# Kernel optimization log

Measured on AMD Instinct MI355X. Metric: run time of the kernel, lower is better.

Reference implementation:

```python
import jax, jax.numpy as jnp
import numpy as np

NEG_SLOPE = 0.2  # PyG GATConv default leaky_relu slope


def _gat_conv(x, src, dst, W, a_src, a_dst, b, num_nodes):
    # Linear transform: [N, F_out]
    h = x @ W
    # Per-node attention halves (heads=1): [N]
    alpha_s = h @ a_src
    alpha_d = h @ a_dst
    # Per-edge raw score for edge j->i: a_src.h_j + a_dst.h_i
    e = jax.nn.leaky_relu(alpha_s[src] + alpha_d[dst], NEG_SLOPE)
    # Softmax over edges grouped by destination node (numerically stable)
    m = jax.ops.segment_max(e, dst, num_segments=num_nodes)
    ex = jnp.exp(e - m[dst])
    denom = jax.ops.segment_sum(ex, dst, num_segments=num_nodes)
    coef = ex / denom[dst]
    # Attention-weighted aggregation of source features into destinations
    out = jax.ops.segment_sum(h[src] * coef[:, None], dst, num_segments=num_nodes)
    return out + b


def setup_inputs() -> dict:
    key = jax.random.key(0)
    ks = jax.random.split(key, 12)
    N, F_in, F_hid, F_out, E = 100000, 128, 64, 40, 1600000
    x = jax.random.normal(ks[0], (N, F_in), dtype=jnp.float32)
    edge_index = jax.random.randint(ks[1], (2, E), 0, N, dtype=jnp.int64)
    g = lambda k, shape, fan: jax.random.normal(k, shape, dtype=jnp.float32) * (1.0 / np.sqrt(fan))
    return {
        "x": x,
        "edge_index": edge_index,
        "W1": g(ks[2], (F_in, F_hid), F_in),
        "a_src1": g(ks[3], (F_hid,), F_hid),
        "a_dst1": g(ks[4], (F_hid,), F_hid),
        "b1": jnp.zeros((F_hid,), dtype=jnp.float32),
        "W2": g(ks[5], (F_hid, F_out), F_hid),
        "a_src2": g(ks[6], (F_out,), F_out),
        "a_dst2": g(ks[7], (F_out,), F_out),
        "b2": jnp.zeros((F_out,), dtype=jnp.float32),
    }


def reference(x, edge_index, W1, a_src1, a_dst1, b1, W2, a_src2, a_dst2, b2):
    N = x.shape[0]
    # PyG GATConv adds self loops by default
    loops = jnp.arange(N, dtype=edge_index.dtype)
    src = jnp.concatenate([edge_index[0], loops])
    dst = jnp.concatenate([edge_index[1], loops])
    h = _gat_conv(x, src, dst, W1, a_src1, a_dst1, b1, N)
    h = jax.nn.relu(h)
    # dropout p=0.5 is inactive in eval mode
    h = _gat_conv(h, src, dst, W2, a_src2, a_dst2, b2, N)
    return jax.nn.log_softmax(h, axis=-1)
```

## Files before the change

### kernel.cpp

```cpp
#include <hip/hip_runtime.h>
#include <math.h>


constexpr int F_IN = 128;
constexpr int F_H  = 64;
constexpr int F_O  = 40;
constexpr int NBMAX = 512;
constexpr int CHUNK = 8192;
constexpr int NKEY  = 2048;

using h2 = decltype(__builtin_amdgcn_cvt_pkrtz(0.f, 0.f));
typedef __attribute__((ext_vector_type(4))) float f32x4;
typedef __attribute__((ext_vector_type(8))) short s16x8;

__device__ __forceinline__ h2 u2h(unsigned u) { return __builtin_bit_cast(h2, u); }

__device__ __forceinline__ float fdot2f(h2 a, h2 b, float c) {
#if __has_builtin(__builtin_amdgcn_fdot2)
    return __builtin_amdgcn_fdot2(a, b, c, false);
#else
    return c + (float)a.x * (float)b.x + (float)a.y * (float)b.y;
#endif
}
__device__ __forceinline__ h2 pklo(unsigned a, unsigned b) {
    return u2h(__builtin_amdgcn_perm(a, b, 0x05040100u));
}
__device__ __forceinline__ h2 pkhi(unsigned a, unsigned b) {
    return u2h(__builtin_amdgcn_perm(a, b, 0x07060302u));
}
__device__ __forceinline__ unsigned short f2h(float f) {
    _Float16 x = (_Float16)f;
    return __builtin_bit_cast(unsigned short, x);
}
__device__ __forceinline__ void nt_storef4(float4* p, float4 v) {
    __builtin_nontemporal_store(v.x, &p->x);
    __builtin_nontemporal_store(v.y, &p->y);
    __builtin_nontemporal_store(v.z, &p->z);
    __builtin_nontemporal_store(v.w, &p->w);
}


__global__ __launch_bounds__(256) void k_binA(const int* __restrict__ dsts,
                                              int* __restrict__ bcnt,
                                              int E, int Et, int NB) {
    __shared__ int hist[NBMAX];
    for (int i = threadIdx.x; i < NB; i += 256) hist[i] = 0;
    __syncthreads();
    int e0 = blockIdx.x * 2048;
#pragma unroll
    for (int it = 0; it < 8; ++it) {
        int e = e0 + it * 256 + threadIdx.x;
        if (e < Et) {
            int d = (e < E) ? dsts[e] : (e - E);
            atomicAdd(&hist[d >> 8], 1);
        }
    }
    __syncthreads();
    for (int i = threadIdx.x; i < NB; i += 256) {
        int c = hist[i];
        if (c) atomicAdd(&bcnt[i], c);
    }
}

__global__ __launch_bounds__(NBMAX) void k_binB(const int* __restrict__ bcnt,
                                                int* __restrict__ bbase,
                                                int* __restrict__ bcur,
                                                int* __restrict__ rp,
                                                int NB, int N, int Et) {
    __shared__ int sc[NBMAX];
    int t = threadIdx.x;
    int v = (t < NB) ? bcnt[t] : 0;
    sc[t] = v; __syncthreads();
    int x = v;
    for (int o = 1; o < NBMAX; o <<= 1) {
        int y = (t >= o) ? sc[t - o] : 0;
        __syncthreads();
        x += y;
        sc[t] = x;
        __syncthreads();
    }
    if (t < NB) { int b = x - v; bbase[t] = b; bcur[t] = b; }
    if (t == 0) rp[N] = Et;
}

__global__ __launch_bounds__(256) void k_binC(const int* __restrict__ srcs,
                                              const int* __restrict__ dsts,
                                              int* __restrict__ bcur,
                                              unsigned* __restrict__ binned,
                                              int E, int Et, int NB) {
    __shared__ int hist[NBMAX];
    __shared__ int gbase[NBMAX];
    __shared__ int lcnt[NBMAX];
    int t = threadIdx.x;
    for (int i = t; i < NB; i += 256) hist[i] = 0;
    __syncthreads();
    int e0 = blockIdx.x * CHUNK;
#pragma unroll 4
    for (int it = 0; it < CHUNK / 256; ++it) {
        int e = e0 + it * 256 + t;
        if (e < Et) {
            int d = (e < E) ? dsts[e] : (e - E);
            atomicAdd(&hist[d >> 8], 1);
        }
    }
    __syncthreads();
    for (int i = t; i < NB; i += 256) {
        int c = hist[i];
        gbase[i] = c ? atomicAdd(&bcur[i], c) : 0;
        lcnt[i] = 0;
    }
    __syncthreads();
#pragma unroll 4
    for (int it = 0; it < CHUNK / 256; ++it) {
        int e = e0 + it * 256 + t;
        if (e < Et) {
            int s, d;
            if (e < E) { s = srcs[e]; d = dsts[e]; } else { s = e - E; d = s; }
            int b = d >> 8;
            int p = atomicAdd(&lcnt[b], 1);
            binned[gbase[b] + p] = (unsigned)s | ((unsigned)(d & 255) << 24);
        }
    }
}


__global__ __launch_bounds__(256) void k_binD(const unsigned* __restrict__ binned,
                                              const int* __restrict__ bbase,
                                              const int* __restrict__ bcur,
                                              int* __restrict__ rp,
                                              int* __restrict__ csr, int N) {
    __shared__ int hist[NKEY];
    __shared__ int sc2[NKEY];
    __shared__ int lcnt[NKEY];
    __shared__ int tsum[256];
    int b = blockIdx.x, t = threadIdx.x;
    int base = bbase[b], end = bcur[b];
    for (int k = t; k < NKEY; k += 256) { hist[k] = 0; lcnt[k] = 0; }
    __syncthreads();
    for (int j = base + t; j < end; j += 256) {
        unsigned w = binned[j];
        int key = ((int)(w >> 24) << 3) | (int)((w & 0xFFFFFFu) >> 14);
        atomicAdd(&hist[key], 1);
    }
    __syncthreads();
    int myk = t << 3;
    int s = 0;
#pragma unroll
    for (int k = 0; k < 8; ++k) s += hist[myk + k];
    tsum[t] = s; __syncthreads();
    int x = s;
    for (int o = 1; o < 256; o <<= 1) {
        int y = (t >= o) ? tsum[t - o] : 0;
        __syncthreads();
        x += y;
        tsum[t] = x;
        __syncthreads();
    }
    int run = x - s;
    int g = (b << 8) + t;
    if (g < N) rp[g] = base + run;
#pragma unroll
    for (int k = 0; k < 8; ++k) { sc2[myk + k] = run; run += hist[myk + k]; }
    __syncthreads();
    for (int j = base + t; j < end; j += 256) {
        unsigned w = binned[j];
        int src = (int)(w & 0xFFFFFFu);
        int key = ((int)(w >> 24) << 3) | (src >> 14);
        int p = atomicAdd(&lcnt[key], 1);
        csr[base + sc2[key] + p] = src;
    }
}


__global__ __launch_bounds__(256) void k_wsplit(const float* __restrict__ W,
                                                unsigned short* __restrict__ WhiT,
                                                unsigned short* __restrict__ WloT) {
    int i = blockIdx.x * 256 + threadIdx.x;
    if (i >= F_IN * F_H) return;
    int k = i >> 6, c = i & 63;
    float w = W[i];
    unsigned u = __float_as_uint(w);
    unsigned hi = u & 0xFFFF0000u;
    float d = w - __uint_as_float(hi);
    WhiT[c * F_IN + k] = (unsigned short)(hi >> 16);
    WloT[c * F_IN + k] = (unsigned short)(__float_as_uint(d) >> 16);
}


__global__ __launch_bounds__(256, 2) void k_gemm1m(const float* __restrict__ x,
                                                   const unsigned short* __restrict__ WhiT,
                                                   const unsigned short* __restrict__ WloT,
                                                   const float* __restrict__ avs,
                                                   const float* __restrict__ avd,
                                                   unsigned short* __restrict__ h,
                                                   float* __restrict__ as,
                                                   float* __restrict__ ad, int N) {
    __shared__ __align__(16) float xs[64][132];
    unsigned short (*hs)[72] = (unsigned short(*)[72])xs;
    const int t = threadIdx.x;
    const int wv = t >> 6;
    const int lane = t & 63;
    const int lrow = lane & 15;
    const int lk8 = lane >> 4;
    const int r0 = blockIdx.x * 64;

    {
        const float4* xg = (const float4*)x;
#pragma unroll
        for (int it = 0; it < 8; ++it) {
            int flat = it * 256 + t;
            int row = flat >> 5, c4 = flat & 31;
            int grow = min(r0 + row, N - 1);
            float4 v = xg[(size_t)grow * 32 + c4];
            *(float4*)&xs[row][c4 * 4] = v;
        }
    }

    s16x8 bh[4][4], bl[4][4];
#pragma unroll
    for (int kt = 0; kt < 4; ++kt)
#pragma unroll
        for (int ct = 0; ct < 4; ++ct) {
            const int boff = (ct * 16 + lrow) * F_IN + kt * 32 + lk8 * 8;
            bh[kt][ct] = *(const s16x8*)&WhiT[boff];
            bl[kt][ct] = *(const s16x8*)&WloT[boff];
        }
    __syncthreads();

    s16x8 ah[4], al[4];
#pragma unroll
    for (int kt = 0; kt < 4; ++kt) {
        const float* rp_ = &xs[wv * 16 + lrow][kt * 32 + lk8 * 8];
        float4 a = *(const float4*)rp_;
        float4 b = *(const float4*)(rp_ + 4);
        float e0[8] = {a.x, a.y, a.z, a.w, b.x, b.y, b.z, b.w};
        unsigned uh[4], ul[4];
#pragma unroll
        for (int p = 0; p < 4; ++p) {
            float a0 = e0[2 * p], a1 = e0[2 * p + 1];
            unsigned u0 = __float_as_uint(a0), u1 = __float_as_uint(a1);
            float d0 = a0 - __uint_as_float(u0 & 0xFFFF0000u);
            float d1 = a1 - __uint_as_float(u1 & 0xFFFF0000u);
            uh[p] = __builtin_amdgcn_perm(u1, u0, 0x07060302u);
            ul[p] = __builtin_amdgcn_perm(__float_as_uint(d1), __float_as_uint(d0), 0x07060302u);
        }
        ah[kt] = __builtin_bit_cast(s16x8, make_uint4(uh[0], uh[1], uh[2], uh[3]));
        al[kt] = __builtin_bit_cast(s16x8, make_uint4(ul[0], ul[1], ul[2], ul[3]));
    }
    __syncthreads();

    f32x4 acc[4] = {};
#pragma unroll
    for (int kt = 0; kt < 4; ++kt) {
#pragma unroll
        for (int ct = 0; ct < 4; ++ct) {
            acc[ct] = __builtin_amdgcn_mfma_f32_16x16x32_bf16(ah[kt], bh[kt][ct], acc[ct], 0, 0, 0);
            acc[ct] = __builtin_amdgcn_mfma_f32_16x16x32_bf16(al[kt], bh[kt][ct], acc[ct], 0, 0, 0);
            acc[ct] = __builtin_amdgcn_mfma_f32_16x16x32_bf16(ah[kt], bl[kt][ct], acc[ct], 0, 0, 0);
        }
    }

    float avs_c[4], avd_c[4];
#pragma unroll
    for (int ct = 0; ct < 4; ++ct) {
        avs_c[ct] = avs[ct * 16 + lrow];
        avd_c[ct] = avd[ct * 16 + lrow];
    }
#pragma unroll
    for (int r = 0; r < 4; ++r) {
        float ps = acc[0][r] * avs_c[0] + acc[1][r] * avs_c[1]
                 + acc[2][r] * avs_c[2] + acc[3][r] * avs_c[3];
        float pd = acc[0][r] * avd_c[0] + acc[1][r] * avd_c[1]
                 + acc[2][r] * avd_c[2] + acc[3][r] * avd_c[3];
#pragma unroll
        for (int o = 8; o; o >>= 1) {
            ps += __shfl_xor(ps, o, 16);
            pd += __shfl_xor(pd, o, 16);
        }
        int orow = r0 + wv * 16 + lk8 * 4 + r;
        if (lrow == 0 && orow < N) { as[orow] = ps; ad[orow] = pd; }
    }

#pragma unroll
    for (int ct = 0; ct < 4; ++ct)
#pragma unroll
        for (int r = 0; r < 4; ++r)
            hs[wv * 16 + lk8 * 4 + r][ct * 16 + lrow] = f2h(acc[ct][r]);
    __syncthreads();
    const int row = t >> 2, ch = t & 3;
    const int grow = r0 + row;
    if (grow < N) {
        uint4 v0 = *(const uint4*)&hs[row][ch * 16];
        uint4 v1 = *(const uint4*)&hs[row][ch * 16 + 8];
        uint4* gp = (uint4*)(h + (size_t)grow * F_H + ch * 16);
        gp[0] = v0; gp[1] = v1;
    }
}


__global__ __launch_bounds__(256) void k_gemm2(const unsigned short* __restrict__ xin,
                                               const float* __restrict__ W,
                                               const float* __restrict__ avs,
                                               const float* __restrict__ avd,
                                               unsigned short* __restrict__ h,
                                               float* __restrict__ as,
                                               float* __restrict__ ad, int N) {
    __shared__ __align__(16) float Ws[F_H * F_O];
    for (int i = threadIdx.x; i < F_H * F_O; i += 256) Ws[i] = W[i];
    __syncthreads();
    int t = threadIdx.x;
    int r0 = blockIdx.x * 64 + (t >> 3) * 2;
    int l = t & 7;
    if (r0 >= N) return;
    const uint2* xa = (const uint2*)(xin + (size_t)r0 * F_H);
    const uint2* xb = (const uint2*)(xin + (size_t)(r0 + 1) * F_H);
    float acca[5] = {}, accb[5] = {};
#pragma unroll
    for (int k4 = 0; k4 < F_H / 4; ++k4) {
        uint2 ua = xa[k4];
        uint2 ub = xb[k4];
        h2 a01 = u2h(ua.x), a23 = u2h(ua.y);
        h2 b01 = u2h(ub.x), b23 = u2h(ub.y);
        float xva[4] = {(float)a01.x, (float)a01.y, (float)a23.x, (float)a23.y};
        float xvb[4] = {(float)b01.x, (float)b01.y, (float)b23.x, (float)b23.y};
        int kb = k4 * 4;
#pragma unroll
        for (int kk = 0; kk < 4; ++kk) {
            const float* wr = &Ws[(kb + kk) * F_O + l];
            float w0 = wr[0], w1 = wr[8], w2 = wr[16], w3 = wr[24], w4 = wr[32];
            float xs = xva[kk];
            acca[0] += xs * w0; acca[1] += xs * w1; acca[2] += xs * w2;
            acca[3] += xs * w3; acca[4] += xs * w4;
            float ys = xvb[kk];
            accb[0] += ys * w0; accb[1] += ys * w1; accb[2] += ys * w2;
            accb[3] += ys * w3; accb[4] += ys * w4;
        }
    }
    float psa = 0.f, pda = 0.f, psb = 0.f, pdb = 0.f;
    unsigned short* ra = h + (size_t)r0 * F_H;
    unsigned short* rb = h + (size_t)(r0 + 1) * F_H;
#pragma unroll
    for (int cc = 0; cc < 5; ++cc) {
        int c = l + 8 * cc;
        ra[c] = f2h(acca[cc]);
        rb[c] = f2h(accb[cc]);
        float vs = avs[c], vd = avd[c];
        psa += acca[cc] * vs; pda += acca[cc] * vd;
        psb += accb[cc] * vs; pdb += accb[cc] * vd;
    }
#pragma unroll
    for (int pp = 0; pp < 3; ++pp) {
        int c = 40 + l * 3 + pp;
        ra[c] = 0; rb[c] = 0;
    }
#pragma unroll
    for (int o = 4; o; o >>= 1) {
        psa += __shfl_xor(psa, o, 8);
        pda += __shfl_xor(pda, o, 8);
        psb += __shfl_xor(psb, o, 8);
        pdb += __shfl_xor(pdb, o, 8);
    }
    if (l == 0) { as[r0] = psa; ad[r0] = pda; as[r0 + 1] = psb; ad[r0 + 1] = pdb; }
}


template <int FOUT, bool RELU, bool LOGSM, bool F16OUT>
__global__ __launch_bounds__(256) void k_agg(const int* __restrict__ rp,
                                             const int* __restrict__ csr,
                                             const float* __restrict__ as,
                                             const float* __restrict__ ad,
                                             const uint4* __restrict__ h4,
                                             const float* __restrict__ bias,
                                             void* __restrict__ outv, int N) {
    constexpr int CAP = 64;
    __shared__ __align__(16) uint2 wsb[4][8][CAP + 2];
    const int w = threadIdx.x >> 6;
    const int g = (threadIdx.x >> 3) & 7;
    const int c = threadIdx.x & 7;
    const int i = blockIdx.x * 32 + (threadIdx.x >> 3);
    if (i >= N) return;
    const int start = rp[i], end = rp[i + 1];
    const int deg = end - start;
    const int dm = min(deg, CAP);
    const int dmR8 = (dm + 7) & ~7;
    const float adi = ad[i];

    for (int idx = c; idx < dm; idx += 8) {
        int srcn = __builtin_nontemporal_load(&csr[start + idx]);
        float e = as[srcn] + adi;
        e = fmaxf(e, 0.2f * e);
        wsb[w][g][idx] = make_uint2(__float_as_uint(__expf(e)), (unsigned)srcn);
    }
    {
        int idx = dm + c;
        if (idx < dmR8) wsb[w][g][idx] = make_uint2(0u, (unsigned)i);
    }

    const uint4* pw = (const uint4*)wsb[w][g];
    float acc[8] = {}, acc2[8] = {};
    float sacc = 0.f;
    const int noct = dmR8 >> 3;
    for (int q = 0; q < noct; ++q) {
        uint4 m0 = pw[4 * q];
        uint4 m1 = pw[4 * q + 1];
        uint4 m2 = pw[4 * q + 2];
        uint4 m3 = pw[4 * q + 3];
        uint4 hv0 = h4[((size_t)m0.y << 3) + c];
        uint4 hv1 = h4[((size_t)m0.w << 3) + c];
        uint4 hv2 = h4[((size_t)m1.y << 3) + c];
        uint4 hv3 = h4[((size_t)m1.w << 3) + c];
        uint4 hv4 = h4[((size_t)m2.y << 3) + c];
        uint4 hv5 = h4[((size_t)m2.w << 3) + c];
        uint4 hv6 = h4[((size_t)m3.y << 3) + c];
        uint4 hv7 = h4[((size_t)m3.w << 3) + c];
        float w0 = __uint_as_float(m0.x), w1 = __uint_as_float(m0.z);
        float w2 = __uint_as_float(m1.x), w3 = __uint_as_float(m1.z);
        float w4 = __uint_as_float(m2.x), w5 = __uint_as_float(m2.z);
        float w6 = __uint_as_float(m3.x), w7 = __uint_as_float(m3.z);
        sacc += ((w0 + w1) + (w2 + w3)) + ((w4 + w5) + (w6 + w7));
        h2 wp0 = __builtin_amdgcn_cvt_pkrtz(w0, w1);
        h2 wp1 = __builtin_amdgcn_cvt_pkrtz(w2, w3);
        h2 wp2 = __builtin_amdgcn_cvt_pkrtz(w4, w5);
        h2 wp3 = __builtin_amdgcn_cvt_pkrtz(w6, w7);
        acc[0] = fdot2f(wp0, pklo(hv1.x, hv0.x), acc[0]);
        acc[1] = fdot2f(wp0, pkhi(hv1.x, hv0.x), acc[1]);
        acc[2] = fdot2f(wp0, pklo(hv1.y, hv0.y), acc[2]);
        acc[3] = fdot2f(wp0, pkhi(hv1.y, hv0.y), acc[3]);
        acc[4] = fdot2f(wp0, pklo(hv1.z, hv0.z), acc[4]);
        acc[5] = fdot2f(wp0, pkhi(hv1.z, hv0.z), acc[5]);
        acc[6] = fdot2f(wp0, pklo(hv1.w, hv0.w), acc[6]);
        acc[7] = fdot2f(wp0, pkhi(hv1.w, hv0.w), acc[7]);
        acc2[0] = fdot2f(wp1, pklo(hv3.x, hv2.x), acc2[0]);
        acc2[1] = fdot2f(wp1, pkhi(hv3.x, hv2.x), acc2[1]);
        acc2[2] = fdot2f(wp1, pklo(hv3.y, hv2.y), acc2[2]);
        acc2[3] = fdot2f(wp1, pkhi(hv3.y, hv2.y), acc2[3]);
        acc2[4] = fdot2f(wp1, pklo(hv3.z, hv2.z), acc2[4]);
        acc2[5] = fdot2f(wp1, pkhi(hv3.z, hv2.z), acc2[5]);
        acc2[6] = fdot2f(wp1, pklo(hv3.w, hv2.w), acc2[6]);
        acc2[7] = fdot2f(wp1, pkhi(hv3.w, hv2.w), acc2[7]);
        acc[0] = fdot2f(wp2, pklo(hv5.x, hv4.x), acc[0]);
        acc[1] = fdot2f(wp2, pkhi(hv5.x, hv4.x), acc[1]);
        acc[2] = fdot2f(wp2, pklo(hv5.y, hv4.y), acc[2]);
        acc[3] = fdot2f(wp2, pkhi(hv5.y, hv4.y), acc[3]);
        acc[4] = fdot2f(wp2, pklo(hv5.z, hv4.z), acc[4]);
        acc[5] = fdot2f(wp2, pkhi(hv5.z, hv4.z), acc[5]);
        acc[6] = fdot2f(wp2, pklo(hv5.w, hv4.w), acc[6]);
        acc[7] = fdot2f(wp2, pkhi(hv5.w, hv4.w), acc[7]);
        acc2[0] = fdot2f(wp3, pklo(hv7.x, hv6.x), acc2[0]);
        acc2[1] = fdot2f(wp3, pkhi(hv7.x, hv6.x), acc2[1]);
        acc2[2] = fdot2f(wp3, pklo(hv7.y, hv6.y), acc2[2]);
        acc2[3] = fdot2f(wp3, pkhi(hv7.y, hv6.y), acc2[3]);
        acc2[4] = fdot2f(wp3, pklo(hv7.z, hv6.z), acc2[4]);
        acc2[5] = fdot2f(wp3, pkhi(hv7.z, hv6.z), acc2[5]);
        acc2[6] = fdot2f(wp3, pklo(hv7.w, hv6.w), acc2[6]);
        acc2[7] = fdot2f(wp3, pkhi(hv7.w, hv6.w), acc2[7]);
    }

    for (int j = start + dm; j < end; ++j) {
        int srcn = __builtin_nontemporal_load(&csr[j]);
        float e = as[srcn] + adi;
        e = fmaxf(e, 0.2f * e);
        float wv = __expf(e);
        sacc += wv;
        uint4 hv = h4[((size_t)srcn << 3) + c];
        h2 wp = __builtin_amdgcn_cvt_pkrtz(wv, 0.f);
        acc[0] = fdot2f(wp, pklo(hv.x, hv.x), acc[0]);
        acc[1] = fdot2f(wp, pkhi(hv.x, hv.x), acc[1]);
        acc[2] = fdot2f(wp, pklo(hv.y, hv.y), acc[2]);
        acc[3] = fdot2f(wp, pkhi(hv.y, hv.y), acc[3]);
        acc[4] = fdot2f(wp, pklo(hv.z, hv.z), acc[4]);
        acc[5] = fdot2f(wp, pkhi(hv.z, hv.z), acc[5]);
        acc[6] = fdot2f(wp, pklo(hv.w, hv.w), acc[6]);
        acc[7] = fdot2f(wp, pkhi(hv.w, hv.w), acc[7]);
    }

#pragma unroll
    for (int k = 0; k < 8; ++k) acc[k] += acc2[k];
    float inv = 1.f / sacc;

    if (!LOGSM) {
        float r[8];
#pragma unroll
        for (int k = 0; k < 8; ++k) {
            r[k] = fmaf(acc[k], inv, bias[8 * c + k]);
            if (RELU) r[k] = fmaxf(r[k], 0.f);
        }
        if (F16OUT) {
            unsigned short* oh = (unsigned short*)outv;
            unsigned u0 = (unsigned)f2h(r[0]) | ((unsigned)f2h(r[1]) << 16);
            unsigned u1 = (unsigned)f2h(r[2]) | ((unsigned)f2h(r[3]) << 16);
            unsigned u2 = (unsigned)f2h(r[4]) | ((unsigned)f2h(r[5]) << 16);
            unsigned u3 = (unsigned)f2h(r[6]) | ((unsigned)f2h(r[7]) << 16);
            *(uint4*)(oh + (size_t)i * F_H + 8 * c) = make_uint4(u0, u1, u2, u3);
        } else {
            float* out = (float*)outv;
            float4* op = (float4*)(out + (size_t)i * FOUT + 8 * c);
            nt_storef4(op, make_float4(r[0], r[1], r[2], r[3]));
            nt_storef4(op + 1, make_float4(r[4], r[5], r[6], r[7]));
        }
    } else {
        float* out = (float*)outv;
        constexpr int VC = FOUT / 8;
        bool act = (c < VC);
        float v[8];
#pragma unroll
        for (int k = 0; k < 8; ++k) {
            float bv = bias[act ? 8 * c + k : 0];
            v[k] = act ? fmaf(acc[k], inv, bv) : -INFINITY;
        }
        float mx = v[0];
#pragma unroll
        for (int k = 1; k < 8; ++k) mx = fmaxf(mx, v[k]);
#pragma unroll
        for (int o = 1; o <= 4; o <<= 1) mx = fmaxf(mx, __shfl_xor(mx, o));
        float es = 0.f;
        if (act) {
#pragma unroll
            for (int k = 0; k < 8; ++k) es += __expf(v[k] - mx);
        }
#pragma unroll
        for (int o = 1; o <= 4; o <<= 1) es += __shfl_xor(es, o);
        if (act) {
            float lse = mx + __logf(es);
            float4* op = (float4*)(out + (size_t)i * FOUT + 8 * c);
            nt_storef4(op, make_float4(v[0] - lse, v[1] - lse, v[2] - lse, v[3] - lse));
            nt_storef4(op + 1, make_float4(v[4] - lse, v[5] - lse, v[6] - lse, v[7] - lse));
        }
    }
}


extern "C" void kernel_launch(void* const* d_in, const int* in_sizes, int n_in,
                              void* d_out, int out_size, void* d_ws, size_t ws_size,
                              hipStream_t stream) {
    const float* x   = (const float*)d_in[0];
    const int* edges = (const int*)d_in[1];
    const float* W1  = (const float*)d_in[2];
    const float* av_s1 = (const float*)d_in[3];
    const float* av_d1 = (const float*)d_in[4];
    const float* b1  = (const float*)d_in[5];
    const float* W2  = (const float*)d_in[6];
    const float* av_s2 = (const float*)d_in[7];
    const float* av_d2 = (const float*)d_in[8];
    const float* b2  = (const float*)d_in[9];
    float* out = (float*)d_out;

    const int N  = in_sizes[0] / F_IN;
    const int E  = in_sizes[1] / 2;
    const int Et = E + N;
    const int NB = (N + 255) >> 8;

    char* p = (char*)d_ws;
    auto alloc = [&](size_t bytes) {
        char* q = p;
        p += (bytes + 255) & ~(size_t)255;
        return (void*)q;
    };
    unsigned short* h1 = (unsigned short*)alloc((size_t)N * F_H * 2);
    unsigned short* out1h = (unsigned short*)alloc((size_t)N * F_H * 2);
    float* as1    = (float*)alloc((size_t)N * 4);
    float* ad1    = (float*)alloc((size_t)N * 4);
    float* as2    = (float*)alloc((size_t)N * 4);
    float* ad2    = (float*)alloc((size_t)N * 4);
    int* rp       = (int*)alloc((size_t)(N + 1) * 4);
    int* bcnt     = (int*)alloc(NBMAX * 4);
    int* bbase    = (int*)alloc(NBMAX * 4);
    int* bcur     = (int*)alloc(NBMAX * 4);
    unsigned* binned = (unsigned*)alloc((size_t)Et * 4);
    int* csr      = (int*)alloc((size_t)Et * 4);
    unsigned short* WhiT = (unsigned short*)alloc((size_t)F_H * F_IN * 2);
    unsigned short* WloT = (unsigned short*)alloc((size_t)F_H * F_IN * 2);
    (void)n_in; (void)out_size; (void)ws_size;

    const int* srcs = edges;
    const int* dsts = edges + E;

    hipMemsetAsync(bcnt, 0, NBMAX * 4, stream);

    k_wsplit<<<(F_IN * F_H + 255) / 256, 256, 0, stream>>>(W1, WhiT, WloT);
    k_binA<<<(Et + 2047) / 2048, 256, 0, stream>>>(dsts, bcnt, E, Et, NB);
    k_binB<<<1, NBMAX, 0, stream>>>(bcnt, bbase, bcur, rp, NB, N, Et);
    k_binC<<<(Et + CHUNK - 1) / CHUNK, 256, 0, stream>>>(srcs, dsts, bcur, binned, E, Et, NB);
    k_binD<<<NB, 256, 0, stream>>>(binned, bbase, bcur, rp, csr, N);

    k_gemm1m<<<(N + 63) / 64, 256, 0, stream>>>(x, WhiT, WloT, av_s1, av_d1, h1, as1, ad1, N);
    int gAgg = (N + 31) / 32;
    k_agg<F_H, true, false, true><<<gAgg, 256, 0, stream>>>(rp, csr, as1, ad1,
                                                            (const uint4*)h1, b1, out1h, N);
    k_gemm2<<<(N + 63) / 64, 256, 0, stream>>>(out1h, W2, av_s2, av_d2, h1, as2, ad2, N);
    k_agg<F_O, false, true, false><<<gAgg, 256, 0, stream>>>(rp, csr, as2, ad2,
                                                             (const uint4*)h1, b2, out, N);
}
```

Before: 292.5 us.

## Fold layer-2 linear transform into aggregation and drop the separate GEMM kernel

```diff
diff --git a/kernel.cpp b/kernel.cpp
--- a/kernel.cpp
+++ b/kernel.cpp
@@ -31,12 +31,6 @@
 __device__ __forceinline__ unsigned short f2h(float f) {
     _Float16 x = (_Float16)f;
     return __builtin_bit_cast(unsigned short, x);
-}
-__device__ __forceinline__ void nt_storef4(float4* p, float4 v) {
-    __builtin_nontemporal_store(v.x, &p->x);
-    __builtin_nontemporal_store(v.y, &p->y);
-    __builtin_nontemporal_store(v.z, &p->z);
-    __builtin_nontemporal_store(v.w, &p->w);
 }
 
 
@@ -187,6 +181,30 @@
 }
 
 
+__global__ __launch_bounds__(64) void k_wprep(const float* __restrict__ W2,
+                                              const float* __restrict__ a2s,
+                                              const float* __restrict__ a2d,
+                                              const float* __restrict__ b2,
+                                              float* __restrict__ wasL,
+                                              float* __restrict__ wadL,
+                                              float* __restrict__ csb) {
+    int k = threadIdx.x;
+    float s = 0.f, d = 0.f;
+    for (int c = 0; c < F_O; ++c) {
+        float w = W2[k * F_O + c];
+        s += w * a2s[c];
+        d += w * a2d[c];
+    }
+    wasL[k] = s;
+    wadL[k] = d;
+    if (k == 0) {
+        float cs = 0.f, cd = 0.f;
+        for (int c = 0; c < F_O; ++c) { cs += b2[c] * a2s[c]; cd += b2[c] * a2d[c]; }
+        csb[0] = cs; csb[1] = cd;
+    }
+}
+
+
 __global__ __launch_bounds__(256, 2) void k_gemm1m(const float* __restrict__ x,
                                                    const unsigned short* __restrict__ WhiT,
                                                    const unsigned short* __restrict__ WloT,
@@ -298,86 +316,37 @@
 }
 
 
-__global__ __launch_bounds__(256) void k_gemm2(const unsigned short* __restrict__ xin,
-                                               const float* __restrict__ W,
-                                               const float* __restrict__ avs,
-                                               const float* __restrict__ avd,
-                                               unsigned short* __restrict__ h,
-                                               float* __restrict__ as,
-                                               float* __restrict__ ad, int N) {
-    __shared__ __align__(16) float Ws[F_H * F_O];
-    for (int i = threadIdx.x; i < F_H * F_O; i += 256) Ws[i] = W[i];
-    __syncthreads();
-    int t = threadIdx.x;
-    int r0 = blockIdx.x * 64 + (t >> 3) * 2;
-    int l = t & 7;
-    if (r0 >= N) return;
-    const uint2* xa = (const uint2*)(xin + (size_t)r0 * F_H);
-    const uint2* xb = (const uint2*)(xin + (size_t)(r0 + 1) * F_H);
-    float acca[5] = {}, accb[5] = {};
-#pragma unroll
-    for (int k4 = 0; k4 < F_H / 4; ++k4) {
-        uint2 ua = xa[k4];
-        uint2 ub = xb[k4];
-        h2 a01 = u2h(ua.x), a23 = u2h(ua.y);
-        h2 b01 = u2h(ub.x), b23 = u2h(ub.y);
-        float xva[4] = {(float)a01.x, (float)a01.y, (float)a23.x, (float)a23.y};
-        float xvb[4] = {(float)b01.x, (float)b01.y, (float)b23.x, (float)b23.y};
-        int kb = k4 * 4;
-#pragma unroll
-        for (int kk = 0; kk < 4; ++kk) {
-            const float* wr = &Ws[(kb + kk) * F_O + l];
-            float w0 = wr[0], w1 = wr[8], w2 = wr[16], w3 = wr[24], w4 = wr[32];
-            float xs = xva[kk];
-            acca[0] += xs * w0; acca[1] += xs * w1; acca[2] += xs * w2;
-            acca[3] += xs * w3; acca[4] += xs * w4;
-            float ys = xvb[kk];
-            accb[0] += ys * w0; accb[1] += ys * w1; accb[2] += ys * w2;
-            accb[3] += ys * w3; accb[4] += ys * w4;
-        }
-    }
-    float psa = 0.f, pda = 0.f, psb = 0.f, pdb = 0.f;
-    unsigned short* ra = h + (size_t)r0 * F_H;
-    unsigned short* rb = h + (size_t)(r0 + 1) * F_H;
-#pragma unroll
-    for (int cc = 0; cc < 5; ++cc) {
-        int c = l + 8 * cc;
-        ra[c] = f2h(acca[cc]);
-        rb[c] = f2h(accb[cc]);
-        float vs = avs[c], vd = avd[c];
-        psa += acca[cc] * vs; pda += acca[cc] * vd;
-        psb += accb[cc] * vs; pdb += accb[cc] * vd;
-    }
-#pragma unroll
-    for (int pp = 0; pp < 3; ++pp) {
-        int c = 40 + l * 3 + pp;
-        ra[c] = 0; rb[c] = 0;
-    }
-#pragma unroll
-    for (int o = 4; o; o >>= 1) {
-        psa += __shfl_xor(psa, o, 8);
-        pda += __shfl_xor(pda, o, 8);
-        psb += __shfl_xor(psb, o, 8);
-        pdb += __shfl_xor(pdb, o, 8);
-    }
-    if (l == 0) { as[r0] = psa; ad[r0] = pda; as[r0 + 1] = psb; ad[r0 + 1] = pdb; }
-}
-
-
-template <int FOUT, bool RELU, bool LOGSM, bool F16OUT>
+template <int MODE>
 __global__ __launch_bounds__(256) void k_agg(const int* __restrict__ rp,
                                              const int* __restrict__ csr,
                                              const float* __restrict__ as,
                                              const float* __restrict__ ad,
                                              const uint4* __restrict__ h4,
-                                             const float* __restrict__ bias,
-                                             void* __restrict__ outv, int N) {
+                                             const float* __restrict__ b1,
+                                             unsigned short* __restrict__ out1h,
+                                             const float* __restrict__ wasL,
+                                             const float* __restrict__ wadL,
+                                             const float* __restrict__ csb,
+                                             float* __restrict__ as2,
+                                             float* __restrict__ ad2,
+                                             const float* __restrict__ W2,
+                                             const float* __restrict__ b2,
+                                             float* __restrict__ out2, int N) {
     constexpr int CAP = 64;
     __shared__ __align__(16) uint2 wsb[4][8][CAP + 2];
-    const int w = threadIdx.x >> 6;
-    const int g = (threadIdx.x >> 3) & 7;
-    const int c = threadIdx.x & 7;
-    const int i = blockIdx.x * 32 + (threadIdx.x >> 3);
+    __shared__ __align__(16) float W2sT[MODE ? F_O * 68 : 1];
+    const int t = threadIdx.x;
+    const int w = t >> 6;
+    const int g = (t >> 3) & 7;
+    const int c = t & 7;
+    if (MODE) {
+        for (int idx = t; idx < F_H * F_O; idx += 256) {
+            int k = idx / F_O, cc = idx - k * F_O;
+            W2sT[cc * 68 + k] = W2[idx];
+        }
+        __syncthreads();
+    }
+    const int i = blockIdx.x * 32 + (t >> 3);
     if (i >= N) return;
     const int start = rp[i], end = rp[i + 1];
     const int deg = end - start;
@@ -478,54 +447,61 @@
     for (int k = 0; k < 8; ++k) acc[k] += acc2[k];
     float inv = 1.f / sacc;
 
-    if (!LOGSM) {
+    if (MODE == 0) {
         float r[8];
 #pragma unroll
-        for (int k = 0; k < 8; ++k) {
-            r[k] = fmaf(acc[k], inv, bias[8 * c + k]);
-            if (RELU) r[k] = fmaxf(r[k], 0.f);
-        }
-        if (F16OUT) {
-            unsigned short* oh = (unsigned short*)outv;
-            unsigned u0 = (unsigned)f2h(r[0]) | ((unsigned)f2h(r[1]) << 16);
-            unsigned u1 = (unsigned)f2h(r[2]) | ((unsigned)f2h(r[3]) << 16);
-            unsigned u2 = (unsigned)f2h(r[4]) | ((unsigned)f2h(r[5]) << 16);
-            unsigned u3 = (unsigned)f2h(r[6]) | ((unsigned)f2h(r[7]) << 16);
-            *(uint4*)(oh + (size_t)i * F_H + 8 * c) = make_uint4(u0, u1, u2, u3);
-        } else {
-            float* out = (float*)outv;
-            float4* op = (float4*)(out + (size_t)i * FOUT + 8 * c);
-            nt_storef4(op, make_float4(r[0], r[1], r[2], r[3]));
-            nt_storef4(op + 1, make_float4(r[4], r[5], r[6], r[7]));
-        }
+        for (int k = 0; k < 8; ++k)
+            r[k] = fmaxf(fmaf(acc[k], inv, b1[8 * c + k]), 0.f);
+        unsigned u0 = (unsigned)f2h(r[0]) | ((unsigned)f2h(r[1]) << 16);
+        unsigned u1 = (unsigned)f2h(r[2]) | ((unsigned)f2h(r[3]) << 16);
+        unsigned u2 = (unsigned)f2h(r[4]) | ((unsigned)f2h(r[5]) << 16);
+        unsigned u3 = (unsigned)f2h(r[6]) | ((unsigned)f2h(r[7]) << 16);
+        *(uint4*)(out1h + (size_t)i * F_H + 8 * c) = make_uint4(u0, u1, u2, u3);
+        float4 wa0 = *(const float4*)&wasL[8 * c];
+        float4 wa1 = *(const float4*)&wasL[8 * c + 4];
+        float4 wd0 = *(const float4*)&wadL[8 * c];
+        float4 wd1 = *(const float4*)&wadL[8 * c + 4];
+        float ps = r[0] * wa0.x + r[1] * wa0.y + r[2] * wa0.z + r[3] * wa0.w
+                 + r[4] * wa1.x + r[5] * wa1.y + r[6] * wa1.z + r[7] * wa1.w;
+        float pd = r[0] * wd0.x + r[1] * wd0.y + r[2] * wd0.z + r[3] * wd0.w
+                 + r[4] * wd1.x + r[5] * wd1.y + r[6] * wd1.z + r[7] * wd1.w;
+#pragma unroll
+        for (int o = 4; o; o >>= 1) {
+            ps += __shfl_xor(ps, o, 8);
+            pd += __shfl_xor(pd, o, 8);
+        }
+        if (c == 0) { as2[i] = ps + csb[0]; ad2[i] = pd + csb[1]; }
     } else {
-        float* out = (float*)outv;
-        constexpr int VC = FOUT / 8;
-        bool act = (c < VC);
-        float v[8];
-#pragma unroll
-        for (int k = 0; k < 8; ++k) {
-            float bv = bias[act ? 8 * c + k : 0];
-            v[k] = act ? fmaf(acc[k], inv, bv) : -INFINITY;
-        }
-        float mx = v[0];
-#pragma unroll
-        for (int k = 1; k < 8; ++k) mx = fmaxf(mx, v[k]);
-#pragma unroll
-        for (int o = 1; o <= 4; o <<= 1) mx = fmaxf(mx, __shfl_xor(mx, o));
-        float es = 0.f;
-        if (act) {
-#pragma unroll
-            for (int k = 0; k < 8; ++k) es += __expf(v[k] - mx);
-        }
-#pragma unroll
-        for (int o = 1; o <= 4; o <<= 1) es += __shfl_xor(es, o);
-        if (act) {
-            float lse = mx + __logf(es);
-            float4* op = (float4*)(out + (size_t)i * FOUT + 8 * c);
-            nt_storef4(op, make_float4(v[0] - lse, v[1] - lse, v[2] - lse, v[3] - lse));
-            nt_storef4(op + 1, make_float4(v[4] - lse, v[5] - lse, v[6] - lse, v[7] - lse));
-        }
+        float* gl = (float*)&wsb[w][g][0];
+        ((float4*)gl)[2 * c]     = make_float4(acc[0] * inv, acc[1] * inv, acc[2] * inv, acc[3] * inv);
+        ((float4*)gl)[2 * c + 1] = make_float4(acc[4] * inv, acc[5] * inv, acc[6] * inv, acc[7] * inv);
+        float v[5];
+#pragma unroll
+        for (int m = 0; m < 5; ++m) v[m] = b2[c + 8 * m];
+#pragma unroll
+        for (int m = 0; m < 5; ++m) {
+            const float* wr = &W2sT[(c + 8 * m) * 68];
+            float vm = v[m];
+#pragma unroll
+            for (int k4 = 0; k4 < 16; ++k4) {
+                float4 a4 = ((const float4*)gl)[k4];
+                float4 w4 = *(const float4*)&wr[k4 * 4];
+                vm += a4.x * w4.x + a4.y * w4.y + a4.z * w4.z + a4.w * w4.w;
+            }
+            v[m] = vm;
+        }
+        float mx = fmaxf(fmaxf(fmaxf(v[0], v[1]), fmaxf(v[2], v[3])), v[4]);
+#pragma unroll
+        for (int o = 4; o; o >>= 1) mx = fmaxf(mx, __shfl_xor(mx, o, 8));
+        float es = __expf(v[0] - mx) + __expf(v[1] - mx) + __expf(v[2] - mx)
+                 + __expf(v[3] - mx) + __expf(v[4] - mx);
+#pragma unroll
+        for (int o = 4; o; o >>= 1) es += __shfl_xor(es, o, 8);
+        float lse = mx + __logf(es);
+        float* op = out2 + (size_t)i * F_O + c;
+#pragma unroll
+        for (int m = 0; m < 5; ++m)
+            __builtin_nontemporal_store(v[m] - lse, op + 8 * m);
     }
 }
 
@@ -570,6 +546,9 @@
     int* csr      = (int*)alloc((size_t)Et * 4);
     unsigned short* WhiT = (unsigned short*)alloc((size_t)F_H * F_IN * 2);
     unsigned short* WloT = (unsigned short*)alloc((size_t)F_H * F_IN * 2);
+    float* wasL   = (float*)alloc(F_H * 4);
+    float* wadL   = (float*)alloc(F_H * 4);
+    float* csb    = (float*)alloc(2 * 4);
     (void)n_in; (void)out_size; (void)ws_size;
 
     const int* srcs = edges;
@@ -578,6 +557,7 @@
     hipMemsetAsync(bcnt, 0, NBMAX * 4, stream);
 
     k_wsplit<<<(F_IN * F_H + 255) / 256, 256, 0, stream>>>(W1, WhiT, WloT);
+    k_wprep<<<1, 64, 0, stream>>>(W2, av_s2, av_d2, b2, wasL, wadL, csb);
     k_binA<<<(Et + 2047) / 2048, 256, 0, stream>>>(dsts, bcnt, E, Et, NB);
     k_binB<<<1, NBMAX, 0, stream>>>(bcnt, bbase, bcur, rp, NB, N, Et);
     k_binC<<<(Et + CHUNK - 1) / CHUNK, 256, 0, stream>>>(srcs, dsts, bcur, binned, E, Et, NB);
@@ -585,9 +565,10 @@
 
     k_gemm1m<<<(N + 63) / 64, 256, 0, stream>>>(x, WhiT, WloT, av_s1, av_d1, h1, as1, ad1, N);
     int gAgg = (N + 31) / 32;
-    k_agg<F_H, true, false, true><<<gAgg, 256, 0, stream>>>(rp, csr, as1, ad1,
-                                                            (const uint4*)h1, b1, out1h, N);
-    k_gemm2<<<(N + 63) / 64, 256, 0, stream>>>(out1h, W2, av_s2, av_d2, h1, as2, ad2, N);
-    k_agg<F_O, false, true, false><<<gAgg, 256, 0, stream>>>(rp, csr, as2, ad2,
-                                                             (const uint4*)h1, b2, out, N);
-}
+    k_agg<0><<<gAgg, 256, 0, stream>>>(rp, csr, as1, ad1, (const uint4*)h1,
+                                       b1, out1h, wasL, wadL, csb, as2, ad2,
+                                       nullptr, nullptr, nullptr, N);
+    k_agg<1><<<gAgg, 256, 0, stream>>>(rp, csr, as2, ad2, (const uint4*)out1h,
+                                       nullptr, nullptr, nullptr, nullptr, nullptr,
+                                       nullptr, nullptr, W2, b2, out, N);
+}
```

Result: faster. 283.1 us (-3.2%).
